# Performance work log

Measured on AMD Instinct MI355X. Metric: run time of the kernel, lower is better.

The kernel has to match this reference:

```python
import jax, jax.numpy as jnp
import numpy as np

EPS = 1e-7

def safe_divide(num, den):
    safe_den = jnp.where(jnp.abs(den) > EPS, den, jnp.sign(den) * EPS)
    return num / safe_den

def mlp(x, W1, b1, W2, b2):
    return jnp.tanh(x @ W1 + b1) @ W2 + b2

B, L, C, H, T = 16384, 256, 512, 1024, 16

def setup_inputs() -> dict:
    key = jax.random.key(0)
    ks = jax.random.split(key, 12)
    s = 0.05
    z = jax.random.normal(ks[0], (B, 2 * L + 1), dtype=jnp.float32)
    ctx = jax.random.normal(ks[1], (B, T, C), dtype=jnp.float32)
    ts = jnp.arange(T, dtype=jnp.float32) * 0.1  # sorted time knots
    t = jnp.float32(0.75)                        # solver query time
    inverse_mass = jnp.ones((1, L), dtype=jnp.float32)
    # fixed diffusion = sqrt(2*gamma/beta), gamma=1, beta=1/3 -> sqrt(6)
    diffusion = jnp.full((1, L), np.sqrt(6.0), dtype=jnp.float32)
    # control_network: Linear(2L+C -> H), tanh, Linear(H -> L)
    Wc1 = jax.random.normal(ks[2], (2 * L + C, H), dtype=jnp.float32) * s
    bc1 = jnp.zeros((H,), dtype=jnp.float32)
    Wc2 = jax.random.normal(ks[3], (H, L), dtype=jnp.float32) * s
    bc2 = jnp.zeros((L,), dtype=jnp.float32)
    # h_net (prior drift): Linear(2L -> H), tanh, Linear(H -> L)
    Wh1 = jax.random.normal(ks[4], (2 * L, H), dtype=jnp.float32) * s
    bh1 = jnp.zeros((H,), dtype=jnp.float32)
    Wh2 = jax.random.normal(ks[5], (H, L), dtype=jnp.float32) * s
    bh2 = jnp.zeros((L,), dtype=jnp.float32)
    return {"z": z, "ts": ts, "t": t, "ctx": ctx,
            "inverse_mass": inverse_mass, "diffusion": diffusion,
            "Wc1": Wc1, "bc1": bc1, "Wc2": Wc2, "bc2": bc2,
            "Wh1": Wh1, "bh1": bh1, "Wh2": Wh2, "bh2": bh2}

def reference(z, ts, t, ctx, inverse_mass, diffusion,
              Wc1, bc1, Wc2, bc2, Wh1, bh1, Wh2, bh2):
    # f_and_g_absolute: one drift/diffusion evaluation of the second-order latent SDE
    pm = z[..., :-1]                      # [B, 2L] position+momentum
    momentum = pm[..., pm.shape[-1] // 2:]  # [B, L]
    # context lookup via searchsorted(right) clamped to last knot
    i = jnp.minimum(jnp.searchsorted(ts, t, side='right'), ts.shape[0] - 1)
    position_drift = inverse_mass * momentum                      # [B, L]
    prior_momentum_drift = mlp(pm, Wh1, bh1, Wh2, bh2)            # [B, L]
    posterior_momentum_drift = mlp(
        jnp.concatenate([pm, ctx[:, i]], axis=-1), Wc1, bc1, Wc2, bc2)  # [B, L]
    difference = prior_momentum_drift - posterior_momentum_drift
    momentum_diffusion = jnp.broadcast_to(diffusion, (z.shape[0], diffusion.shape[-1]))
    dkl_drift = jnp.sum(jnp.square(safe_divide(difference, momentum_diffusion)),
                        axis=-1, keepdims=True)                   # [B, 1]
    drift = jnp.concatenate([position_drift, posterior_momentum_drift, dkl_drift], axis=-1)
    diffusion_out = jnp.concatenate(
        [jnp.zeros_like(momentum_diffusion), momentum_diffusion,
         jnp.zeros_like(dkl_drift)], axis=-1)
    return drift, diffusion_out
```

## Files before the change

### kernel.cpp

```cpp
#include <hip/hip_runtime.h>

typedef __attribute__((ext_vector_type(8))) short short8;
typedef __attribute__((ext_vector_type(4))) float f32x4;

#define AS1 __attribute__((address_space(1)))
#define AS3 __attribute__((address_space(3)))

#define NB 16384
#define LDIM 256
#define CDIM 512
#define HDIM 1024

__device__ __forceinline__ unsigned short f2bf(float x) {
    unsigned u = __float_as_uint(x);
    u += 0x7fffu + ((u >> 16) & 1u);
    return (unsigned short)(u >> 16);
}

__device__ __forceinline__ void gld_lds16(const unsigned short* g, unsigned short* l) {
    __builtin_amdgcn_global_load_lds((const AS1 void*)g, (AS3 void*)l, 16, 0, 0);
}

__device__ __forceinline__ float tanh_fast(float x) {
    x = fminf(fmaxf(x, -15.f), 15.f);
    float e = __expf(2.f * x);
    return (e - 1.f) / (e + 1.f);
}

__global__ void build_w(const float* __restrict__ Wc1, const float* __restrict__ bc1,
                        const float* __restrict__ Wc2, const float* __restrict__ bc2,
                        const float* __restrict__ Wh1, const float* __restrict__ bh1,
                        const float* __restrict__ Wh2, const float* __restrict__ bh2,
                        unsigned short* __restrict__ W1T, unsigned short* __restrict__ W2T,
                        float* __restrict__ bias1, float* __restrict__ bias2)
{
    const int R1 = 2048 * 1024;
    const int R2 = R1 + 512 * 1024;
    const int R3 = R2 + 2048;
    const int R4 = R3 + 512;
    int id = blockIdx.x * 256 + threadIdx.x;
    if (id < R1) {
        int n = id >> 10, k = id & 1023;
        float v;
        if (n < 1024) v = Wc1[k * 1024 + n];
        else          v = (k < 512) ? Wh1[k * 1024 + (n - 1024)] : 0.f;
        W1T[id] = f2bf(v);
    } else if (id < R2) {
        int id2 = id - R1;
        int n = id2 >> 10, k = id2 & 1023;
        float v = (n < 256) ? Wc2[k * 256 + n] : Wh2[k * 256 + (n - 256)];
        W2T[id2] = f2bf(v);
    } else if (id < R3) {
        int n = id - R2;
        bias1[n] = (n < 1024) ? bc1[n] : bh1[n - 1024];
    } else if (id < R4) {
        int n = id - R3;
        bias2[n] = (n < 256) ? bc2[n] : bh2[n - 256];
    }
}

__global__ void build_A1(const float* __restrict__ z, const float* __restrict__ ts,
                         const float* __restrict__ t, const float* __restrict__ ctx,
                         unsigned short* __restrict__ A1)
{
    __shared__ int sh_i;
    if (threadIdx.x == 0) {
        float tv = t[0];
        int c = 0;
        #pragma unroll
        for (int q = 0; q < 16; ++q) c += (ts[q] <= tv) ? 1 : 0;
        sh_i = (c < 15) ? c : 15;
    }
    __syncthreads();
    const int i = sh_i;
    size_t id = (size_t)blockIdx.x * 256 + threadIdx.x;
    int b = (int)(id >> 10);
    int col = (int)(id & 1023);
    float v = (col < 512) ? z[(size_t)b * 513 + col]
                          : ctx[((size_t)b * 16 + i) * 512 + (col - 512)];
    A1[id] = f2bf(v);
}

template<int LAYER>
__global__ __launch_bounds__(256)
void gemm_tile(const unsigned short* __restrict__ A, const unsigned short* __restrict__ BT,
               const float* __restrict__ bias,
               unsigned short* __restrict__ Hout, float* __restrict__ Fout)
{
    __shared__ unsigned short sA[128 * 32];
    __shared__ unsigned short sB[128 * 32];

    const int tid  = threadIdx.x;
    const int lane = tid & 63;
    const int wave = tid >> 6;
    const int ntile = blockIdx.x;
    const int mtile = blockIdx.y;

    int lda, aoff, kdim;
    if (LAYER == 1) { lda = 1024; aoff = 0;                       kdim = (ntile < 8) ? 1024 : 512; }
    else            { lda = 2048; aoff = (ntile < 2) ? 0 : 1024;  kdim = 1024; }

    const int m0 = mtile * 128;
    const int n0 = ntile * 128;

    const int row0 = tid >> 2,         cb0 = tid & 3;
    const int row1 = (256 + tid) >> 2, cb1 = (256 + tid) & 3;

    const unsigned short* aG0 = A + (size_t)(m0 + row0) * lda + aoff + cb0 * 8;
    const unsigned short* aG1 = A + (size_t)(m0 + row1) * lda + aoff + cb1 * 8;
    const unsigned short* bG0 = BT + (size_t)(n0 + row0) * 1024 + cb0 * 8;
    const unsigned short* bG1 = BT + (size_t)(n0 + row1) * 1024 + cb1 * 8;

    unsigned short* sA0 = sA + (size_t)(wave * 64) * 8;
    unsigned short* sA1 = sA + (size_t)(256 + wave * 64) * 8;
    unsigned short* sB0 = sB + (size_t)(wave * 64) * 8;
    unsigned short* sB1 = sB + (size_t)(256 + wave * 64) * 8;

    const int wm = (wave & 1) * 64;
    const int wn = (wave >> 1) * 64;
    const int lr = lane & 15;
    const int kq = (lane >> 4) * 8;

    f32x4 acc[4][4] = {};

    for (int k0 = 0; k0 < kdim; k0 += 32) {
        gld_lds16(aG0 + k0, sA0);
        gld_lds16(aG1 + k0, sA1);
        gld_lds16(bG0 + k0, sB0);
        gld_lds16(bG1 + k0, sB1);
        __syncthreads();

        short8 af[4], bfr[4];
        #pragma unroll
        for (int i = 0; i < 4; ++i)
            af[i] = *(const short8*)&sA[(wm + i * 16 + lr) * 32 + kq];
        #pragma unroll
        for (int i = 0; i < 4; ++i)
            bfr[i] = *(const short8*)&sB[(wn + i * 16 + lr) * 32 + kq];

        #pragma unroll
        for (int i = 0; i < 4; ++i)
            #pragma unroll
            for (int j = 0; j < 4; ++j)
                acc[i][j] = __builtin_amdgcn_mfma_f32_16x16x32_bf16(af[i], bfr[j], acc[i][j], 0, 0, 0);
        __syncthreads();
    }

    const int rquad = (lane >> 4) * 4;
    #pragma unroll
    for (int i = 0; i < 4; ++i) {
        const int gr = m0 + wm + i * 16 + rquad;
        #pragma unroll
        for (int j = 0; j < 4; ++j) {
            const int gc = n0 + wn + j * 16 + lr;
            const float bs = bias[gc];
            #pragma unroll
            for (int r = 0; r < 4; ++r) {
                float x = acc[i][j][r] + bs;
                if (LAYER == 1) {
                    Hout[(size_t)(gr + r) * 2048 + gc] = f2bf(tanh_fast(x));
                } else {
                    Fout[(size_t)(gr + r) * 512 + gc] = x;
                }
            }
        }
    }
}

__global__ void finalize(const float* __restrict__ z,
                         const float* __restrict__ inverse_mass,
                         const float* __restrict__ diffusion,
                         const float* __restrict__ PR,
                         float* __restrict__ out)
{
    const int b = blockIdx.x;
    const int j = threadIdx.x;

    float mom  = z[(size_t)b * 513 + 256 + j];
    float pd   = inverse_mass[j] * mom;
    float post = PR[(size_t)b * 512 + j];
    float pri  = PR[(size_t)b * 512 + 256 + j];
    float d    = diffusion[j];
    float sgn  = (d > 0.f) ? 1.f : ((d < 0.f) ? -1.f : 0.f);
    float sd   = (fabsf(d) > 1e-7f) ? d : sgn * 1e-7f;
    float q    = (pri - post) / sd;
    float sq   = q * q;

    #pragma unroll
    for (int off = 32; off > 0; off >>= 1) sq += __shfl_down(sq, off, 64);
    __shared__ float ws4[4];
    if ((j & 63) == 0) ws4[j >> 6] = sq;
    __syncthreads();

    float* drift = out + (size_t)b * 513;
    float* dif   = out + (size_t)NB * 513 + (size_t)b * 513;
    drift[j]       = pd;
    drift[256 + j] = post;
    dif[j]         = 0.f;
    dif[256 + j]   = d;
    if (j == 0) {
        drift[512] = ws4[0] + ws4[1] + ws4[2] + ws4[3];
        dif[512]   = 0.f;
    }
}

extern "C" void kernel_launch(void* const* d_in, const int* in_sizes, int n_in,
                              void* d_out, int out_size, void* d_ws, size_t ws_size,
                              hipStream_t stream) {
    const float* z    = (const float*)d_in[0];
    const float* ts   = (const float*)d_in[1];
    const float* t    = (const float*)d_in[2];
    const float* ctx  = (const float*)d_in[3];
    const float* im   = (const float*)d_in[4];
    const float* dfu  = (const float*)d_in[5];
    const float* Wc1  = (const float*)d_in[6];
    const float* bc1  = (const float*)d_in[7];
    const float* Wc2  = (const float*)d_in[8];
    const float* bc2  = (const float*)d_in[9];
    const float* Wh1  = (const float*)d_in[10];
    const float* bh1  = (const float*)d_in[11];
    const float* Wh2  = (const float*)d_in[12];
    const float* bh2  = (const float*)d_in[13];

    char* ws = (char*)d_ws;
    unsigned short* A1  = (unsigned short*)(ws);
    unsigned short* H   = (unsigned short*)(ws + 33554432ull);
    unsigned short* W1T = (unsigned short*)(ws + 100663296ull);
    unsigned short* W2T = (unsigned short*)(ws + 104857600ull);
    float*          b1  = (float*)(ws + 105906176ull);
    float*          b2  = (float*)(ws + 105914368ull);
    float*          PR  = (float*)(ws + 105916416ull);

    build_w<<<10250, 256, 0, stream>>>(Wc1, bc1, Wc2, bc2, Wh1, bh1, Wh2, bh2, W1T, W2T, b1, b2);
    build_A1<<<65536, 256, 0, stream>>>(z, ts, t, ctx, A1);

    dim3 g1(16, 128);
    gemm_tile<1><<<g1, 256, 0, stream>>>(A1, W1T, b1, H, nullptr);
    dim3 g2(4, 128);
    gemm_tile<2><<<g2, 256, 0, stream>>>(H, W2T, b2, nullptr, PR);

    finalize<<<NB, 256, 0, stream>>>(z, im, dfu, PR, (float*)d_out);
}
```

Baseline: 824.2 us.

## Fuse finalize into second GEMM epilogue, vectorize A1 build, swizzle tile order

The second GEMM now computes posterior and prior outputs for the same rows and columns in one block. It writes drift and diffusion straight to the output and accumulates the KL term with atomics, so the PR round trip and the separate finalize kernel go away. build_A1 now handles eight elements per thread with vector loads and stores, and it zeroes the KL accumulator slots. Both GEMMs remap block indices to group neighbouring tiles, aiming for better L2 reuse. The risks are that the atomic summation order is nondeterministic and that the fused epilogue writes output with scattered, uncoalesced stores.

```diff
diff --git a/kernel.cpp b/kernel.cpp
--- a/kernel.cpp
+++ b/kernel.cpp
@@ -61,7 +61,7 @@
 
 __global__ void build_A1(const float* __restrict__ z, const float* __restrict__ ts,
                          const float* __restrict__ t, const float* __restrict__ ctx,
-                         unsigned short* __restrict__ A1)
+                         unsigned short* __restrict__ A1, float* __restrict__ out)
 {
     __shared__ int sh_i;
     if (threadIdx.x == 0) {
@@ -74,18 +74,29 @@
     __syncthreads();
     const int i = sh_i;
     size_t id = (size_t)blockIdx.x * 256 + threadIdx.x;
-    int b = (int)(id >> 10);
-    int col = (int)(id & 1023);
-    float v = (col < 512) ? z[(size_t)b * 513 + col]
-                          : ctx[((size_t)b * 16 + i) * 512 + (col - 512)];
-    A1[id] = f2bf(v);
-}
-
-template<int LAYER>
+    int b  = (int)(id >> 7);
+    int c0 = ((int)id & 127) << 3;
+    short8 v;
+    if (c0 < 512) {
+        const float* zp = z + (size_t)b * 513 + c0;
+        #pragma unroll
+        for (int q = 0; q < 8; ++q) v[q] = (short)f2bf(zp[q]);
+    } else {
+        const f32x4* cp = (const f32x4*)(ctx + ((size_t)b * 16 + i) * 512 + (c0 - 512));
+        f32x4 x0 = cp[0], x1 = cp[1];
+        #pragma unroll
+        for (int q = 0; q < 4; ++q) { v[q] = (short)f2bf(x0[q]); v[4 + q] = (short)f2bf(x1[q]); }
+    }
+    *(short8*)(A1 + id * 8) = v;
+    if (id < NB) {
+        out[id * 513 + 512] = 0.f;
+        out[(size_t)NB * 513 + id * 513 + 512] = 0.f;
+    }
+}
+
 __global__ __launch_bounds__(256)
-void gemm_tile(const unsigned short* __restrict__ A, const unsigned short* __restrict__ BT,
-               const float* __restrict__ bias,
-               unsigned short* __restrict__ Hout, float* __restrict__ Fout)
+void gemm1(const unsigned short* __restrict__ A, const unsigned short* __restrict__ BT,
+           const float* __restrict__ bias, unsigned short* __restrict__ Hout)
 {
     __shared__ unsigned short sA[128 * 32];
     __shared__ unsigned short sB[128 * 32];
@@ -93,12 +104,12 @@
     const int tid  = threadIdx.x;
     const int lane = tid & 63;
     const int wave = tid >> 6;
-    const int ntile = blockIdx.x;
-    const int mtile = blockIdx.y;
-
-    int lda, aoff, kdim;
-    if (LAYER == 1) { lda = 1024; aoff = 0;                       kdim = (ntile < 8) ? 1024 : 512; }
-    else            { lda = 2048; aoff = (ntile < 2) ? 0 : 1024;  kdim = 1024; }
+
+    int lin = blockIdx.y * 16 + blockIdx.x;
+    lin = (lin & 7) * 256 + (lin >> 3);
+    const int ntile = lin & 15;
+    const int mtile = lin >> 4;
+    const int kdim  = (ntile < 8) ? 1024 : 512;
 
     const int m0 = mtile * 128;
     const int n0 = ntile * 128;
@@ -106,8 +117,8 @@
     const int row0 = tid >> 2,         cb0 = tid & 3;
     const int row1 = (256 + tid) >> 2, cb1 = (256 + tid) & 3;
 
-    const unsigned short* aG0 = A + (size_t)(m0 + row0) * lda + aoff + cb0 * 8;
-    const unsigned short* aG1 = A + (size_t)(m0 + row1) * lda + aoff + cb1 * 8;
+    const unsigned short* aG0 = A + (size_t)(m0 + row0) * 1024 + cb0 * 8;
+    const unsigned short* aG1 = A + (size_t)(m0 + row1) * 1024 + cb1 * 8;
     const unsigned short* bG0 = BT + (size_t)(n0 + row0) * 1024 + cb0 * 8;
     const unsigned short* bG1 = BT + (size_t)(n0 + row1) * 1024 + cb1 * 8;
 
@@ -157,50 +168,125 @@
             #pragma unroll
             for (int r = 0; r < 4; ++r) {
                 float x = acc[i][j][r] + bs;
-                if (LAYER == 1) {
-                    Hout[(size_t)(gr + r) * 2048 + gc] = f2bf(tanh_fast(x));
-                } else {
-                    Fout[(size_t)(gr + r) * 512 + gc] = x;
-                }
+                Hout[(size_t)(gr + r) * 2048 + gc] = f2bf(tanh_fast(x));
             }
         }
     }
 }
 
-__global__ void finalize(const float* __restrict__ z,
-                         const float* __restrict__ inverse_mass,
-                         const float* __restrict__ diffusion,
-                         const float* __restrict__ PR,
-                         float* __restrict__ out)
+__global__ __launch_bounds__(256)
+void gemm2_fused(const unsigned short* __restrict__ Hm, const unsigned short* __restrict__ W2T,
+                 const float* __restrict__ bias2, const float* __restrict__ z,
+                 const float* __restrict__ im, const float* __restrict__ dfu,
+                 float* __restrict__ out)
 {
-    const int b = blockIdx.x;
-    const int j = threadIdx.x;
-
-    float mom  = z[(size_t)b * 513 + 256 + j];
-    float pd   = inverse_mass[j] * mom;
-    float post = PR[(size_t)b * 512 + j];
-    float pri  = PR[(size_t)b * 512 + 256 + j];
-    float d    = diffusion[j];
-    float sgn  = (d > 0.f) ? 1.f : ((d < 0.f) ? -1.f : 0.f);
-    float sd   = (fabsf(d) > 1e-7f) ? d : sgn * 1e-7f;
-    float q    = (pri - post) / sd;
-    float sq   = q * q;
-
+    __shared__ unsigned short sAp[64 * 32];
+    __shared__ unsigned short sAq[64 * 32];
+    __shared__ unsigned short sBp[128 * 32];
+    __shared__ unsigned short sBq[128 * 32];
+
+    const int tid  = threadIdx.x;
+    const int lane = tid & 63;
+    const int wave = tid >> 6;
+
+    int lin = blockIdx.y * 2 + blockIdx.x;
+    lin = (lin & 7) * 64 + (lin >> 3);
+    const int n0 = (lin & 1) * 128;
+    const int m0 = (lin >> 1) * 64;
+
+    const int arow = tid >> 2, acb = tid & 3;
+    const int brow1 = (256 + tid) >> 2, bcb1 = (256 + tid) & 3;
+
+    const unsigned short* aGp  = Hm  + (size_t)(m0 + arow) * 2048 + acb * 8;
+    const unsigned short* aGq  = aGp + 1024;
+    const unsigned short* bGp0 = W2T + (size_t)(n0 + arow) * 1024 + acb * 8;
+    const unsigned short* bGp1 = W2T + (size_t)(n0 + brow1) * 1024 + bcb1 * 8;
+    const unsigned short* bGq0 = bGp0 + 256 * 1024;
+    const unsigned short* bGq1 = bGp1 + 256 * 1024;
+
+    unsigned short* dAp  = sAp + wave * 512;
+    unsigned short* dAq  = sAq + wave * 512;
+    unsigned short* dBp0 = sBp + wave * 512;
+    unsigned short* dBp1 = sBp + 2048 + wave * 512;
+    unsigned short* dBq0 = sBq + wave * 512;
+    unsigned short* dBq1 = sBq + 2048 + wave * 512;
+
+    const int wn = wave * 32;
+    const int lr = lane & 15;
+    const int kq = (lane >> 4) * 8;
+
+    f32x4 accp[4][2] = {};
+    f32x4 accq[4][2] = {};
+
+    for (int k0 = 0; k0 < 1024; k0 += 32) {
+        gld_lds16(aGp  + k0, dAp);
+        gld_lds16(aGq  + k0, dAq);
+        gld_lds16(bGp0 + k0, dBp0);
+        gld_lds16(bGp1 + k0, dBp1);
+        gld_lds16(bGq0 + k0, dBq0);
+        gld_lds16(bGq1 + k0, dBq1);
+        __syncthreads();
+
+        short8 afp[4], afq[4], bp[2], bq[2];
+        #pragma unroll
+        for (int i = 0; i < 4; ++i) {
+            afp[i] = *(const short8*)&sAp[(i * 16 + lr) * 32 + kq];
+            afq[i] = *(const short8*)&sAq[(i * 16 + lr) * 32 + kq];
+        }
+        #pragma unroll
+        for (int j = 0; j < 2; ++j) {
+            bp[j] = *(const short8*)&sBp[(wn + j * 16 + lr) * 32 + kq];
+            bq[j] = *(const short8*)&sBq[(wn + j * 16 + lr) * 32 + kq];
+        }
+
+        #pragma unroll
+        for (int i = 0; i < 4; ++i)
+            #pragma unroll
+            for (int j = 0; j < 2; ++j) {
+                accp[i][j] = __builtin_amdgcn_mfma_f32_16x16x32_bf16(afp[i], bp[j], accp[i][j], 0, 0, 0);
+                accq[i][j] = __builtin_amdgcn_mfma_f32_16x16x32_bf16(afq[i], bq[j], accq[i][j], 0, 0, 0);
+            }
+        __syncthreads();
+    }
+
+    const int rquad = (lane >> 4) * 4;
+    float bcv[2], bhv[2], dv[2], sdv[2], imv[2];
     #pragma unroll
-    for (int off = 32; off > 0; off >>= 1) sq += __shfl_down(sq, off, 64);
-    __shared__ float ws4[4];
-    if ((j & 63) == 0) ws4[j >> 6] = sq;
-    __syncthreads();
-
-    float* drift = out + (size_t)b * 513;
-    float* dif   = out + (size_t)NB * 513 + (size_t)b * 513;
-    drift[j]       = pd;
-    drift[256 + j] = post;
-    dif[j]         = 0.f;
-    dif[256 + j]   = d;
-    if (j == 0) {
-        drift[512] = ws4[0] + ws4[1] + ws4[2] + ws4[3];
-        dif[512]   = 0.f;
+    for (int j = 0; j < 2; ++j) {
+        const int gc = n0 + wn + j * 16 + lr;
+        bcv[j] = bias2[gc];
+        bhv[j] = bias2[256 + gc];
+        float d = dfu[gc];
+        dv[j] = d;
+        float sgn = (d > 0.f) ? 1.f : ((d < 0.f) ? -1.f : 0.f);
+        sdv[j] = (fabsf(d) > 1e-7f) ? d : sgn * 1e-7f;
+        imv[j] = im[gc];
+    }
+
+    #pragma unroll
+    for (int i = 0; i < 4; ++i) {
+        #pragma unroll
+        for (int r = 0; r < 4; ++r) {
+            const int gr = m0 + i * 16 + rquad + r;
+            float* drift = out + (size_t)gr * 513;
+            float* dif   = out + (size_t)NB * 513 + (size_t)gr * 513;
+            float s2 = 0.f;
+            #pragma unroll
+            for (int j = 0; j < 2; ++j) {
+                const int gc = n0 + wn + j * 16 + lr;
+                float post = accp[i][j][r] + bcv[j];
+                float pri  = accq[i][j][r] + bhv[j];
+                drift[256 + gc] = post;
+                drift[gc]       = imv[j] * z[(size_t)gr * 513 + 256 + gc];
+                dif[gc]         = 0.f;
+                dif[256 + gc]   = dv[j];
+                float qq = (pri - post) / sdv[j];
+                s2 += qq * qq;
+            }
+            #pragma unroll
+            for (int m = 1; m < 16; m <<= 1) s2 += __shfl_xor(s2, m, 64);
+            if (lr == 0) atomicAdd(&drift[512], s2);
+        }
     }
 }
 
@@ -229,15 +315,15 @@
     unsigned short* W2T = (unsigned short*)(ws + 104857600ull);
     float*          b1  = (float*)(ws + 105906176ull);
     float*          b2  = (float*)(ws + 105914368ull);
-    float*          PR  = (float*)(ws + 105916416ull);
+
+    float* out = (float*)d_out;
 
     build_w<<<10250, 256, 0, stream>>>(Wc1, bc1, Wc2, bc2, Wh1, bh1, Wh2, bh2, W1T, W2T, b1, b2);
-    build_A1<<<65536, 256, 0, stream>>>(z, ts, t, ctx, A1);
+    build_A1<<<8192, 256, 0, stream>>>(z, ts, t, ctx, A1, out);
 
     dim3 g1(16, 128);
-    gemm_tile<1><<<g1, 256, 0, stream>>>(A1, W1T, b1, H, nullptr);
-    dim3 g2(4, 128);
-    gemm_tile<2><<<g2, 256, 0, stream>>>(H, W2T, b2, nullptr, PR);
-
-    finalize<<<NB, 256, 0, stream>>>(z, im, dfu, PR, (float*)d_out);
-}
+    gemm1<<<g1, 256, 0, stream>>>(A1, W1T, b1, H);
+
+    dim3 g2(2, 256);
+    gemm2_fused<<<g2, 256, 0, stream>>>(H, W2T, b2, z, im, dfu, out);
+}
```

Result: faster. 805.6 us (-2.3%).
